# Kernel optimization log

Hardware: AMD Instinct MI355X
Metric: run time of the kernel (lower is better)

The kernel has to match this reference:

```python
import jax, jax.numpy as jnp
import numpy as np

K = 0.5            # init kwarg k (score threshold)
G, S, C, M, DE = 256, 128, 512, 384, 128
N = G * S          # total nodes
EG = S + M         # edges per graph (first S point at the graph's last 'super' node)
E = G * EG


def setup_inputs() -> dict:
    key = jax.random.key(0)
    ks = jax.random.split(key, 8)
    x = jax.random.normal(ks[0], (N, C), jnp.float32)
    W = jax.random.normal(ks[1], (1, C), jnp.float32)
    batch = jnp.repeat(jnp.arange(G, dtype=jnp.int32), S)
    edge_num = jnp.full((G,), EG, dtype=jnp.int32)
    off = jnp.arange(G, dtype=jnp.int32) * S
    # structured edges: node i -> last node of its graph (the 'super node')
    struct_src = off[:, None] + jnp.arange(S, dtype=jnp.int32)[None, :]
    struct_dst = jnp.broadcast_to((off + S - 1)[:, None], (G, S))
    rand_src = jax.random.randint(ks[2], (G, M), 0, S, jnp.int32) + off[:, None]
    rand_dst = jax.random.randint(ks[3], (G, M), 0, S, jnp.int32) + off[:, None]
    src = jnp.concatenate([struct_src, rand_src], axis=1).reshape(-1)
    dst = jnp.concatenate([struct_dst, rand_dst], axis=1).reshape(-1)
    edge_index = jnp.stack([src, dst], axis=0)  # [2, E], grouped per graph
    edge_inform = jax.random.normal(ks[4], (E, DE), jnp.float32)
    br_feature = jax.random.normal(ks[5], (N, C), jnp.float32)
    return dict(x=x, edge_index=edge_index, edge_num=edge_num, edge_inform=edge_inform,
                batch=batch, br_feature=br_feature, br_index=edge_index,
                br_batch=batch, br_com_num=jnp.zeros((G,), jnp.int32), W=W)


def reference(x, edge_index, edge_num, edge_inform, batch, br_feature, br_index, br_batch, br_com_num, W):
    n, e, g = x.shape[0], edge_index.shape[1], edge_num.shape[0]
    score = jax.nn.sigmoid(jnp.mean(x * W, axis=-1))          # [N]
    x_out = x * score[:, None] * 2.0

    # per-graph node layout
    counts = jnp.bincount(batch, length=g)
    node_off = jnp.cumsum(counts) - counts
    last_node = node_off + counts - 1                          # 'super node' of each graph
    is_last = jnp.zeros((n,), bool).at[last_node].set(True)
    # torch loop runs over all but the last node of each graph
    low = (score < K) & (~is_last)                             # [N]

    # per-graph edge layout
    e_graph = jnp.repeat(jnp.arange(g, dtype=edge_num.dtype), edge_num)
    e_off = jnp.cumsum(edge_num) - edge_num
    local_pos = jnp.arange(e) - e_off[e_graph]                 # position inside graph's slice
    src, dst = edge_index[0], edge_index[1]
    # torch searches positions [1, eg) backwards for edge (low_node -> last_node): the
    # LAST matching position per low-score node gets masked out.
    cand = (dst == last_node[e_graph]) & low[src] & (batch[src] == e_graph) & (local_pos >= 1)
    val = jnp.where(cand, jnp.arange(e), -1)
    rem = jax.ops.segment_max(val, src, num_segments=n)        # last candidate edge per node
    drop = rem[rem >= 0]
    edge_mask = jnp.ones((e,), bool).at[drop].set(False)

    edge_num_plus = jax.ops.segment_sum(edge_mask.astype(edge_num.dtype), e_graph, num_segments=g)
    edge_index_plus = edge_index[:, edge_mask]
    edge_inform_plus = edge_inform[edge_mask]

    # BatchReversal: remove node (local_low_idx + com_num[g] + br_node_offset[g]) per low node
    n2 = br_feature.shape[0]
    counts2 = jnp.bincount(br_batch, length=g)
    node_off2 = jnp.cumsum(counts2) - counts2
    low_nodes = jnp.arange(n)[low]
    g_of = batch[low_nodes]
    br_drop = (low_nodes - node_off[g_of]) + br_com_num[g_of] + node_off2[g_of]
    br_mask = jnp.ones((n2,), bool).at[br_drop].set(False)
    leave = jnp.arange(n2)[br_mask]

    # filter_edge: keep nodes, remap edge endpoints, drop dangling edges
    br_feature_p = br_feature[leave]
    br_batch_p = br_batch[leave]
    remap = jnp.full((n2,), -1, dtype=jnp.int32).at[leave].set(jnp.arange(leave.shape[0], dtype=jnp.int32))
    r, c = remap[br_index[0]], remap[br_index[1]]
    keep = (r >= 0) & (c >= 0)
    br_index_p = jnp.stack([r[keep], c[keep]], axis=0)

    return (x_out, edge_index_plus, edge_inform_plus, edge_num_plus,
            br_feature_p, br_index_p, br_batch_p)
```

## Files before the change

### kernel.cpp

```cpp
#include <hip/hip_runtime.h>
#include <math.h>


__global__ void k_count_both(const int* __restrict__ batch, int N,
                             const int* __restrict__ br_batch, int N2,
                             int* __restrict__ counts, int* __restrict__ counts2){
  int i = blockIdx.x*blockDim.x + threadIdx.x;
  if (i < N) atomicAdd(&counts[batch[i]], 1);
  else if (i < N + N2) atomicAdd(&counts2[br_batch[i - N]], 1);
}

__device__ void scan512_excl(const int* __restrict__ in, int* __restrict__ out,
                             int G, int* s){
  int t = threadIdx.x;
  int v = (t < G) ? in[t] : 0;
  s[t] = v; __syncthreads();
  for (int off = 1; off < 512; off <<= 1){
    int add = (t >= off) ? s[t - off] : 0;
    __syncthreads();
    s[t] += add;
    __syncthreads();
  }
  if (t < G) out[t] = s[t] - v;
  __syncthreads();
}

__global__ void k_scanG(const int* __restrict__ counts, const int* __restrict__ counts2,
                        const int* __restrict__ edge_num, int G,
                        int* __restrict__ node_off, int* __restrict__ node_off2,
                        int* __restrict__ e_off){
  __shared__ int s[512];
  scan512_excl(counts,  node_off,  G, s);
  scan512_excl(counts2, node_off2, G, s);
  scan512_excl(edge_num, e_off,    G, s);
}

__global__ void __launch_bounds__(256) k_score(
    const float* __restrict__ x, const float* __restrict__ W,
    const int* __restrict__ batch, const int* __restrict__ counts,
    const int* __restrict__ node_off,
    float* __restrict__ out_x, int* __restrict__ low, int* __restrict__ rem,
    int C, int N){
  int wave = (blockIdx.x * blockDim.x + threadIdx.x) >> 6;
  int lane = threadIdx.x & 63;
  if (wave >= N) return;
  const float4* x4 = (const float4*)(x + (size_t)wave * C);
  const float4* W4 = (const float4*)W;
  const int nv = C >> 2;
  float4 vals[8];
  float acc = 0.f;
  int m = 0;
  for (int k = lane; k < nv; k += 64){
    float4 a = x4[k]; float4 w = W4[k];
    acc += a.x*w.x + a.y*w.y + a.z*w.z + a.w*w.w;
    if (m < 8) vals[m] = a;
    m++;
  }
  #pragma unroll
  for (int d = 1; d < 64; d <<= 1) acc += __shfl_xor(acc, d, 64);
  float scale = 2.0f / (1.0f + expf(-acc / (float)C));
  if (lane == 0){
    int g    = batch[wave];
    int last = node_off[g] + counts[g] - 1;
    low[wave] = (acc < 0.0f) && (wave != last) ? 1 : 0;
    rem[wave] = -1;
  }
  float4* o4 = (float4*)(out_x + (size_t)wave * C);
  m = 0;
  for (int k = lane; k < nv; k += 64){
    float4 a = (m < 8) ? vals[m] : x4[k];
    m++;
    a.x *= scale; a.y *= scale; a.z *= scale; a.w *= scale;
    o4[k] = a;
  }
}

__device__ __forceinline__ int find_graph(const int* __restrict__ e_off, int G, int e){
  int lo = 0, hi = G - 1;
  while (lo < hi){
    int mid = (lo + hi + 1) >> 1;
    if (e_off[mid] <= e) lo = mid; else hi = mid - 1;
  }
  return lo;
}

__global__ void k_pass1(const int* __restrict__ ei, const int* __restrict__ e_off,
                        const int* __restrict__ node_off, const int* __restrict__ node_off2,
                        const int* __restrict__ counts, const int* __restrict__ batch,
                        const int* __restrict__ low, const int* __restrict__ br_com_num,
                        int* __restrict__ rem, int* __restrict__ brmask,
                        int E, int N, int G){
  int e = blockIdx.x*blockDim.x + threadIdx.x;
  if (e < N && low[e]){
    int g = batch[e];
    int d = e - node_off[g] + br_com_num[g] + node_off2[g];
    brmask[d] = 1;
  }
  if (e >= E) return;
  int g  = find_graph(e_off, G, e);
  if (e - e_off[g] < 1) return;
  int dst  = ei[E + e];
  int last = node_off[g] + counts[g] - 1;
  if (dst != last) return;
  int src = ei[e];
  if (!low[src]) return;
  if (batch[src] != g) return;
  atomicMax(&rem[src], e);
}

__global__ void k_pass2(const int* __restrict__ ei, const int* __restrict__ rem,
                        const int* __restrict__ e_off, const int* __restrict__ brmask,
                        int* __restrict__ dropcnt,
                        int* __restrict__ bsumsA, int* __restrict__ bsumsB,
                        int E, int N2, int G, int nbE){
  __shared__ int s[256];
  int b = blockIdx.x, t = threadIdx.x;
  int v = 0;
  if (b < nbE){
    int e = b*256 + t;
    if (e < E){
      v = (rem[ei[e]] != e) ? 1 : 0;
      if (!v){ int g = find_graph(e_off, G, e); atomicAdd(&dropcnt[g], 1); }
    }
  } else {
    int j = (b - nbE)*256 + t;
    v = (j < N2) ? (brmask[j] == 0) : 0;
  }
  s[t] = v; __syncthreads();
  for (int off = 128; off > 0; off >>= 1){
    if (t < off) s[t] += s[t + off];
    __syncthreads();
  }
  if (t == 0){
    if (b < nbE) bsumsA[b] = s[0];
    else         bsumsB[b - nbE] = s[0];
  }
}

__device__ void scan_bsums_dev(int* __restrict__ bsums, int nb, int* __restrict__ total){
  __shared__ int s[1024];
  int t = threadIdx.x;
  int v = (t < nb) ? bsums[t] : 0;
  s[t] = v; __syncthreads();
  for (int off = 1; off < 1024; off <<= 1){
    int add = (t >= off) ? s[t - off] : 0;
    __syncthreads();
    s[t] += add;
    __syncthreads();
  }
  if (t < nb)      bsums[t] = s[t] - v;
  if (t == nb - 1) *total   = s[t];
}

__global__ void k_scanAB(int* __restrict__ bsumsA, int nbA,
                         int* __restrict__ bsumsB, int nbB,
                         int* __restrict__ totals){
  if (blockIdx.x == 0) scan_bsums_dev(bsumsA, nbA, &totals[0]);
  else                 scan_bsums_dev(bsumsB, nbB, &totals[1]);
}

__global__ void k_scanC(int* __restrict__ bsumsC, int nb, int* __restrict__ totals){
  scan_bsums_dev(bsumsC, nb, &totals[2]);
}

__device__ __forceinline__ int excl_scan256(int v, int* s){
  int t = threadIdx.x;
  s[t] = v; __syncthreads();
  for (int off = 1; off < 256; off <<= 1){
    int add = (t >= off) ? s[t - off] : 0;
    __syncthreads();
    s[t] += add;
    __syncthreads();
  }
  return s[t] - v;
}

__global__ void k_pass3(const int* __restrict__ ei, const int* __restrict__ rem,
                        const int* __restrict__ bsumsA, const int* __restrict__ bsumsB,
                        const int* __restrict__ totals,
                        const int* __restrict__ edge_num, const int* __restrict__ dropcnt,
                        const int* __restrict__ brmask,
                        int* __restrict__ edge_pos, int* __restrict__ remap,
                        float* __restrict__ out, long long base0,
                        int E, int N2, int G, int DE, int nbE){
  __shared__ int s[256];
  int b = blockIdx.x, t = threadIdx.x;
  if (b < nbE){
    int e = b*256 + t;
    int keep = 0, src = 0, dst = 0;
    if (e < E){ src = ei[e]; dst = ei[E + e]; keep = (rem[src] != e) ? 1 : 0; }
    int excl = excl_scan256(keep, s);
    long long ek = totals[0];
    if (e < E){
      if (keep){
        int p = bsumsA[b] + excl;
        edge_pos[e] = p;
        out[base0 + p]      = (float)src;
        out[base0 + ek + p] = (float)dst;
      } else edge_pos[e] = -1;
    }
    if (b == 0){
      long long off3 = base0 + 2*ek + ek*(long long)DE;
      for (int g = t; g < G; g += 256)
        out[off3 + g] = (float)(edge_num[g] - dropcnt[g]);
    }
  } else {
    int j = (b - nbE)*256 + t;
    int keep = (j < N2) ? (brmask[j] == 0) : 0;
    int excl = excl_scan256(keep, s);
    if (j < N2) remap[j] = keep ? (bsumsB[b - nbE] + excl) : -1;
  }
}

__global__ void __launch_bounds__(256) k_pass4(
    const int* __restrict__ bi, const int* __restrict__ remap,
    const float* __restrict__ inform, const int* __restrict__ edge_pos,
    const int* __restrict__ totals,
    int* __restrict__ bsumsC, float* __restrict__ out,
    long long base0, int EB, int E, int DE, int nbB){
  int b = blockIdx.x, t = threadIdx.x;
  if (b < nbB){
    __shared__ int s[256];
    int e = b*256 + t;
    int v = 0;
    if (e < EB) v = (remap[bi[e]] >= 0 && remap[bi[EB + e]] >= 0) ? 1 : 0;
    s[t] = v; __syncthreads();
    for (int off = 128; off > 0; off >>= 1){
      if (t < off) s[t] += s[t + off];
      __syncthreads();
    }
    if (t == 0) bsumsC[b] = s[0];
  } else {
    int e = (b - nbB)*8 + (t >> 5);
    if (e >= E) return;
    int p = edge_pos[e];
    if (p < 0) return;
    long long ek   = totals[0];
    long long off2 = base0 + 2*ek;
    int lane = t & 31;
    const float4* in4 = (const float4*)(inform + (size_t)e * DE);
    float4*       o4  = (float4*)(out + off2 + (long long)p * DE);
    for (int j = lane; j < (DE >> 2); j += 32) o4[j] = in4[j];
  }
}

__global__ void __launch_bounds__(256) k_pass5(
    const int* __restrict__ bi, const int* __restrict__ remap,
    const int* __restrict__ bsumsC, const int* __restrict__ totals,
    const float* __restrict__ brf, const int* __restrict__ brb,
    float* __restrict__ out, long long base0,
    int G, int DE, int C, int EB, int N2, int nbB){
  int b = blockIdx.x, t = threadIdx.x;
  long long ek = totals[0], nk = totals[1], kc = totals[2];
  long long off4 = base0 + 2*ek + ek*(long long)DE + G;
  if (b < nbB){
    __shared__ int s[256];
    int e = b*256 + t;
    int r = -1, c = -1, keep = 0;
    if (e < EB){
      r = remap[bi[e]];
      c = remap[bi[EB + e]];
      keep = (r >= 0 && c >= 0) ? 1 : 0;
    }
    int excl = excl_scan256(keep, s);
    if (keep){
      long long off5 = off4 + nk*(long long)C;
      int p = bsumsC[b] + excl;
      out[off5 + p]      = (float)r;
      out[off5 + kc + p] = (float)c;
    }
  } else {
    int j = (b - nbB)*2 + (t >> 7);
    if (j >= N2) return;
    int p = remap[j];
    if (p < 0) return;
    int lane = t & 127;
    const float4* in4 = (const float4*)(brf + (size_t)j * C);
    float4*       o4  = (float4*)(out + off4 + (long long)p * C);
    for (int k = lane; k < (C >> 2); k += 128) o4[k] = in4[k];
    if (lane == 0){
      long long off6 = off4 + nk*(long long)C + 2*kc;
      out[off6 + p] = (float)brb[j];
    }
  }
}

extern "C" void kernel_launch(void* const* d_in, const int* in_sizes, int n_in,
                              void* d_out, int out_size, void* d_ws, size_t ws_size,
                              hipStream_t stream){
  const float* x           = (const float*)d_in[0];
  const int*   edge_index  = (const int*)  d_in[1];
  const int*   edge_num    = (const int*)  d_in[2];
  const float* edge_inform = (const float*)d_in[3];
  const int*   batch       = (const int*)  d_in[4];
  const float* br_feature  = (const float*)d_in[5];
  const int*   br_index    = (const int*)  d_in[6];
  const int*   br_batch    = (const int*)  d_in[7];
  const int*   br_com_num  = (const int*)  d_in[8];
  const float* W           = (const float*)d_in[9];
  float* out = (float*)d_out;

  const int C  = in_sizes[9];
  const int N  = in_sizes[4];
  const int G  = in_sizes[2];
  const int E  = in_sizes[1] / 2;
  const int DE = in_sizes[3] / E;
  const int N2 = in_sizes[7];
  const int EB = in_sizes[6] / 2;

  int* ws        = (int*)d_ws;
  int* counts    = ws;
  int* counts2   = counts    + G;
  int* dropcnt   = counts2   + G;
  int* brmask    = dropcnt   + G;
  int* node_off  = brmask    + N2;
  int* node_off2 = node_off  + G;
  int* e_off     = node_off2 + G;
  int* totals    = e_off     + G;
  int* low       = totals    + 8;
  int* rem       = low       + N;
  int* remap     = rem       + N;
  int* edge_pos  = remap     + N2;
  int* bsumsA    = edge_pos  + E;
  int* bsumsB    = bsumsA    + 1024;
  int* bsumsC    = bsumsB    + 1024;

  const long long base0 = (long long)N * C;

  const int nbN2 = (N2 + 255) / 256;
  const int nbE  = (E  + 255) / 256;
  const int nbB  = (EB + 255) / 256;

  hipMemsetAsync(counts, 0, sizeof(int) * (3 * (size_t)G + N2), stream);

  k_count_both<<<(N + N2 + 255) / 256, 256, 0, stream>>>(batch, N, br_batch, N2,
                                                         counts, counts2);
  k_scanG<<<1, 512, 0, stream>>>(counts, counts2, edge_num, G,
                                 node_off, node_off2, e_off);

  k_score<<<(N * 64 + 255) / 256, 256, 0, stream>>>(x, W, batch, counts, node_off,
                                                    out, low, rem, C, N);

  k_pass1<<<(max(E, N) + 255) / 256, 256, 0, stream>>>(
      edge_index, e_off, node_off, node_off2, counts, batch, low, br_com_num,
      rem, brmask, E, N, G);

  k_pass2<<<nbE + nbN2, 256, 0, stream>>>(edge_index, rem, e_off, brmask,
                                          dropcnt, bsumsA, bsumsB,
                                          E, N2, G, nbE);

  k_scanAB<<<2, 1024, 0, stream>>>(bsumsA, nbE, bsumsB, nbN2, totals);

  k_pass3<<<nbE + nbN2, 256, 0, stream>>>(edge_index, rem, bsumsA, bsumsB, totals,
                                          edge_num, dropcnt, brmask,
                                          edge_pos, remap, out, base0,
                                          E, N2, G, DE, nbE);

  k_pass4<<<nbB + (E + 7) / 8, 256, 0, stream>>>(br_index, remap,
                                                 edge_inform, edge_pos, totals,
                                                 bsumsC, out, base0,
                                                 EB, E, DE, nbB);

  k_scanC<<<1, 1024, 0, stream>>>(bsumsC, nbB, totals);

  k_pass5<<<nbB + (N2 + 1) / 2, 256, 0, stream>>>(br_index, remap, bsumsC, totals,
                                                  br_feature, br_batch, out, base0,
                                                  G, DE, C, EB, N2, nbB);
}
```

Measured before the change: 423.3 us.

## Fuse prep kernels and move br-edge count into pass2 to cut launches

Replaces the memset, counting and scan kernels with one single-block prep kernel that counts in shared memory and zeroes dropcnt and brmask. The br-edge keep count now reads brmask directly in pass2, so its block-sum scan joins the A/B scan kernel and pass4/pass5 merge into one launch. This removes several launches and serial dependencies. The cost is that one 512-thread block serially walks all N and N2 entries for counting and zeroing, which may be slow.

```diff
diff --git a/kernel.cpp b/kernel.cpp
--- a/kernel.cpp
+++ b/kernel.cpp
@@ -2,18 +2,8 @@
 #include <math.h>
 
 
-__global__ void k_count_both(const int* __restrict__ batch, int N,
-                             const int* __restrict__ br_batch, int N2,
-                             int* __restrict__ counts, int* __restrict__ counts2){
-  int i = blockIdx.x*blockDim.x + threadIdx.x;
-  if (i < N) atomicAdd(&counts[batch[i]], 1);
-  else if (i < N + N2) atomicAdd(&counts2[br_batch[i - N]], 1);
-}
-
-__device__ void scan512_excl(const int* __restrict__ in, int* __restrict__ out,
-                             int G, int* s){
+__device__ __forceinline__ int scan512_excl_val(int v, int* s){
   int t = threadIdx.x;
-  int v = (t < G) ? in[t] : 0;
   s[t] = v; __syncthreads();
   for (int off = 1; off < 512; off <<= 1){
     int add = (t >= off) ? s[t - off] : 0;
@@ -21,18 +11,39 @@
     s[t] += add;
     __syncthreads();
   }
-  if (t < G) out[t] = s[t] - v;
+  int r = s[t] - v;
   __syncthreads();
-}
-
-__global__ void k_scanG(const int* __restrict__ counts, const int* __restrict__ counts2,
-                        const int* __restrict__ edge_num, int G,
-                        int* __restrict__ node_off, int* __restrict__ node_off2,
-                        int* __restrict__ e_off){
-  __shared__ int s[512];
-  scan512_excl(counts,  node_off,  G, s);
-  scan512_excl(counts2, node_off2, G, s);
-  scan512_excl(edge_num, e_off,    G, s);
+  return r;
+}
+
+__global__ void __launch_bounds__(512) k_prep(
+    const int* __restrict__ batch, int N,
+    const int* __restrict__ br_batch, int N2,
+    const int* __restrict__ edge_num, int G,
+    int* __restrict__ counts, int* __restrict__ counts2,
+    int* __restrict__ node_off, int* __restrict__ node_off2,
+    int* __restrict__ e_off,
+    int* __restrict__ dropcnt, int* __restrict__ brmask){
+  __shared__ int c1[512], c2[512], s[512];
+  int t = threadIdx.x;
+  c1[t] = 0; c2[t] = 0;
+  __syncthreads();
+  for (int i = t; i < N;  i += 512) atomicAdd(&c1[batch[i]], 1);
+  for (int i = t; i < N2; i += 512) atomicAdd(&c2[br_batch[i]], 1);
+  for (int i = t; i < G;  i += 512) dropcnt[i] = 0;
+  for (int i = t; i < N2; i += 512) brmask[i] = 0;
+  __syncthreads();
+  int v1 = (t < G) ? c1[t] : 0;
+  int v2 = (t < G) ? c2[t] : 0;
+  int v3 = (t < G) ? edge_num[t] : 0;
+  int o1 = scan512_excl_val(v1, s);
+  int o2 = scan512_excl_val(v2, s);
+  int o3 = scan512_excl_val(v3, s);
+  if (t < G){
+    counts[t]  = v1;  node_off[t]  = o1;
+    counts2[t] = v2;  node_off2[t] = o2;
+    e_off[t]   = o3;
+  }
 }
 
 __global__ void __launch_bounds__(256) k_score(
@@ -110,9 +121,11 @@
 
 __global__ void k_pass2(const int* __restrict__ ei, const int* __restrict__ rem,
                         const int* __restrict__ e_off, const int* __restrict__ brmask,
+                        const int* __restrict__ bi,
                         int* __restrict__ dropcnt,
                         int* __restrict__ bsumsA, int* __restrict__ bsumsB,
-                        int E, int N2, int G, int nbE){
+                        int* __restrict__ bsumsC,
+                        int E, int N2, int EB, int G, int nbE, int nbN2){
   __shared__ int s[256];
   int b = blockIdx.x, t = threadIdx.x;
   int v = 0;
@@ -122,9 +135,13 @@
       v = (rem[ei[e]] != e) ? 1 : 0;
       if (!v){ int g = find_graph(e_off, G, e); atomicAdd(&dropcnt[g], 1); }
     }
-  } else {
+  } else if (b < nbE + nbN2){
     int j = (b - nbE)*256 + t;
     v = (j < N2) ? (brmask[j] == 0) : 0;
+  } else {
+    int e = (b - nbE - nbN2)*256 + t;
+    if (e < EB)
+      v = (brmask[bi[e]] == 0 && brmask[bi[EB + e]] == 0) ? 1 : 0;
   }
   s[t] = v; __syncthreads();
   for (int off = 128; off > 0; off >>= 1){
@@ -132,8 +149,9 @@
     __syncthreads();
   }
   if (t == 0){
-    if (b < nbE) bsumsA[b] = s[0];
-    else         bsumsB[b - nbE] = s[0];
+    if (b < nbE)            bsumsA[b] = s[0];
+    else if (b < nbE + nbN2) bsumsB[b - nbE] = s[0];
+    else                     bsumsC[b - nbE - nbN2] = s[0];
   }
 }
 
@@ -152,15 +170,13 @@
   if (t == nb - 1) *total   = s[t];
 }
 
-__global__ void k_scanAB(int* __restrict__ bsumsA, int nbA,
-                         int* __restrict__ bsumsB, int nbB,
-                         int* __restrict__ totals){
-  if (blockIdx.x == 0) scan_bsums_dev(bsumsA, nbA, &totals[0]);
-  else                 scan_bsums_dev(bsumsB, nbB, &totals[1]);
-}
-
-__global__ void k_scanC(int* __restrict__ bsumsC, int nb, int* __restrict__ totals){
-  scan_bsums_dev(bsumsC, nb, &totals[2]);
+__global__ void k_scanABC(int* __restrict__ bsumsA, int nbA,
+                          int* __restrict__ bsumsB, int nbB,
+                          int* __restrict__ bsumsC, int nbC,
+                          int* __restrict__ totals){
+  if      (blockIdx.x == 0) scan_bsums_dev(bsumsA, nbA, &totals[0]);
+  else if (blockIdx.x == 1) scan_bsums_dev(bsumsB, nbB, &totals[1]);
+  else                      scan_bsums_dev(bsumsC, nbC, &totals[2]);
 }
 
 __device__ __forceinline__ int excl_scan256(int v, int* s){
@@ -212,49 +228,20 @@
   }
 }
 
-__global__ void __launch_bounds__(256) k_pass4(
+__global__ void __launch_bounds__(256) k_pass45(
     const int* __restrict__ bi, const int* __restrict__ remap,
+    const int* __restrict__ bsumsC, const int* __restrict__ totals,
     const float* __restrict__ inform, const int* __restrict__ edge_pos,
-    const int* __restrict__ totals,
-    int* __restrict__ bsumsC, float* __restrict__ out,
-    long long base0, int EB, int E, int DE, int nbB){
+    const float* __restrict__ brf, const int* __restrict__ brb,
+    float* __restrict__ out, long long base0,
+    int G, int DE, int C, int EB, int E, int N2,
+    int nbB, int nbE8){
   int b = blockIdx.x, t = threadIdx.x;
+  long long ek = totals[0];
   if (b < nbB){
     __shared__ int s[256];
-    int e = b*256 + t;
-    int v = 0;
-    if (e < EB) v = (remap[bi[e]] >= 0 && remap[bi[EB + e]] >= 0) ? 1 : 0;
-    s[t] = v; __syncthreads();
-    for (int off = 128; off > 0; off >>= 1){
-      if (t < off) s[t] += s[t + off];
-      __syncthreads();
-    }
-    if (t == 0) bsumsC[b] = s[0];
-  } else {
-    int e = (b - nbB)*8 + (t >> 5);
-    if (e >= E) return;
-    int p = edge_pos[e];
-    if (p < 0) return;
-    long long ek   = totals[0];
-    long long off2 = base0 + 2*ek;
-    int lane = t & 31;
-    const float4* in4 = (const float4*)(inform + (size_t)e * DE);
-    float4*       o4  = (float4*)(out + off2 + (long long)p * DE);
-    for (int j = lane; j < (DE >> 2); j += 32) o4[j] = in4[j];
-  }
-}
-
-__global__ void __launch_bounds__(256) k_pass5(
-    const int* __restrict__ bi, const int* __restrict__ remap,
-    const int* __restrict__ bsumsC, const int* __restrict__ totals,
-    const float* __restrict__ brf, const int* __restrict__ brb,
-    float* __restrict__ out, long long base0,
-    int G, int DE, int C, int EB, int N2, int nbB){
-  int b = blockIdx.x, t = threadIdx.x;
-  long long ek = totals[0], nk = totals[1], kc = totals[2];
-  long long off4 = base0 + 2*ek + ek*(long long)DE + G;
-  if (b < nbB){
-    __shared__ int s[256];
+    long long nk = totals[1], kc = totals[2];
+    long long off4 = base0 + 2*ek + ek*(long long)DE + G;
     int e = b*256 + t;
     int r = -1, c = -1, keep = 0;
     if (e < EB){
@@ -269,8 +256,20 @@
       out[off5 + p]      = (float)r;
       out[off5 + kc + p] = (float)c;
     }
+  } else if (b < nbB + nbE8){
+    int e = (b - nbB)*8 + (t >> 5);
+    if (e >= E) return;
+    int p = edge_pos[e];
+    if (p < 0) return;
+    long long off2 = base0 + 2*ek;
+    int lane = t & 31;
+    const float4* in4 = (const float4*)(inform + (size_t)e * DE);
+    float4*       o4  = (float4*)(out + off2 + (long long)p * DE);
+    for (int j = lane; j < (DE >> 2); j += 32) o4[j] = in4[j];
   } else {
-    int j = (b - nbB)*2 + (t >> 7);
+    long long nk = totals[1], kc = totals[2];
+    long long off4 = base0 + 2*ek + ek*(long long)DE + G;
+    int j = (b - nbB - nbE8)*2 + (t >> 7);
     if (j >= N2) return;
     int p = remap[j];
     if (p < 0) return;
@@ -330,13 +329,11 @@
   const int nbN2 = (N2 + 255) / 256;
   const int nbE  = (E  + 255) / 256;
   const int nbB  = (EB + 255) / 256;
-
-  hipMemsetAsync(counts, 0, sizeof(int) * (3 * (size_t)G + N2), stream);
-
-  k_count_both<<<(N + N2 + 255) / 256, 256, 0, stream>>>(batch, N, br_batch, N2,
-                                                         counts, counts2);
-  k_scanG<<<1, 512, 0, stream>>>(counts, counts2, edge_num, G,
-                                 node_off, node_off2, e_off);
+  const int nbE8 = (E + 7) / 8;
+
+  k_prep<<<1, 512, 0, stream>>>(batch, N, br_batch, N2, edge_num, G,
+                                counts, counts2, node_off, node_off2, e_off,
+                                dropcnt, brmask);
 
   k_score<<<(N * 64 + 255) / 256, 256, 0, stream>>>(x, W, batch, counts, node_off,
                                                     out, low, rem, C, N);
@@ -345,25 +342,21 @@
       edge_index, e_off, node_off, node_off2, counts, batch, low, br_com_num,
       rem, brmask, E, N, G);
 
-  k_pass2<<<nbE + nbN2, 256, 0, stream>>>(edge_index, rem, e_off, brmask,
-                                          dropcnt, bsumsA, bsumsB,
-                                          E, N2, G, nbE);
-
-  k_scanAB<<<2, 1024, 0, stream>>>(bsumsA, nbE, bsumsB, nbN2, totals);
+  k_pass2<<<nbE + nbN2 + nbB, 256, 0, stream>>>(edge_index, rem, e_off, brmask,
+                                                br_index, dropcnt,
+                                                bsumsA, bsumsB, bsumsC,
+                                                E, N2, EB, G, nbE, nbN2);
+
+  k_scanABC<<<3, 1024, 0, stream>>>(bsumsA, nbE, bsumsB, nbN2, bsumsC, nbB,
+                                    totals);
 
   k_pass3<<<nbE + nbN2, 256, 0, stream>>>(edge_index, rem, bsumsA, bsumsB, totals,
                                           edge_num, dropcnt, brmask,
                                           edge_pos, remap, out, base0,
                                           E, N2, G, DE, nbE);
 
-  k_pass4<<<nbB + (E + 7) / 8, 256, 0, stream>>>(br_index, remap,
-                                                 edge_inform, edge_pos, totals,
-                                                 bsumsC, out, base0,
-                                                 EB, E, DE, nbB);
-
-  k_scanC<<<1, 1024, 0, stream>>>(bsumsC, nbB, totals);
-
-  k_pass5<<<nbB + (N2 + 1) / 2, 256, 0, stream>>>(br_index, remap, bsumsC, totals,
-                                                  br_feature, br_batch, out, base0,
-                                                  G, DE, C, EB, N2, nbB);
-}
+  k_pass45<<<nbB + nbE8 + (N2 + 1) / 2, 256, 0, stream>>>(
+      br_index, remap, bsumsC, totals, edge_inform, edge_pos,
+      br_feature, br_batch, out, base0,
+      G, DE, C, EB, E, N2, nbB, nbE8);
+}
```

Measured after the change: 425.6 us. About the same (+0.5%).
